# Kernel tuning notes

Measured on AMD Instinct MI355X. Metric: run time of the kernel, lower is better.

The kernel has to match this reference:

```python
import jax, jax.numpy as jnp
import numpy as np

NFILTS = 6  # module-level global in the original repo


def setup_inputs() -> dict:
    key = jax.random.key(0)
    k = jax.random.split(key, 6)
    N, T, D, E = 128, 256, 10, NFILTS
    merged = jax.random.normal(k[0], (N, T, 14), dtype=jnp.float32)
    y_pred_i = jax.random.normal(k[1], (N, T, E), dtype=jnp.float32)
    y_pred_ij = jax.random.normal(k[2], (N, N, T, E), dtype=jnp.float32)
    # input1 holds flux errors in channels [1+nfilts : -2]; keep them bounded away from 0
    input1 = jax.random.uniform(k[3], (N, T, 1 + E + E + 2), dtype=jnp.float32) + 0.5
    samples = jax.random.normal(k[4], (N, D), dtype=jnp.float32)
    labels = jax.random.randint(k[5], (N,), 0, 10, dtype=jnp.int64)
    return {"merged": merged, "y_pred_i": y_pred_i, "y_pred_ij": y_pred_ij,
            "input1": input1, "samples": samples, "labels": labels}


def reference(merged, y_pred_i, y_pred_ij, input1, samples, labels):
    # err_true: [N, T, E]
    err_true = input1[:, :, 1 + NFILTS:-2]
    # pairwise latent distance: S_ij[i,j] = mean_d (samples[j] - samples[i])^2 -> [N, N]
    d = samples[None, :, :] - samples[:, None, :]
    S_ij = jnp.mean(d * d, axis=-1)
    # second term: mean over (T, E) of (y_pred_ij[i,j] - y_pred_i[j])^2 / err_true[j]^2 / 10
    diffsq = jnp.square(y_pred_ij - y_pred_i[None, :, :, :])          # [N, N, T, E]
    second = jnp.mean(diffsq / jnp.square(err_true)[None], axis=(2, 3)) / 10.0  # [N, N]
    avg_term = 0.5 * (second + second.T)
    L_sim = jnp.mean(jnp.abs(S_ij - avg_term))
    return L_sim
```

## Files before the change

kernel.cpp:

```cpp
#include <hip/hip_runtime.h>

#define NN 128
#define TT 256
#define EE 6
#define DD 10
#define TE (TT*EE)
#define C1 15

typedef float f32x4 __attribute__((ext_vector_type(4)));

__global__ __launch_bounds__(256) void pair_all(const float* __restrict__ yij,
                                                const float* __restrict__ yi,
                                                const float* __restrict__ input1,
                                                float* __restrict__ raw,
                                                float* __restrict__ out) {
    const int bid = blockIdx.x;
    const int tid = threadIdx.x;
    const int j   = bid & (NN - 1);

    if (bid == 0 && tid == 0) out[0] = 0.0f;

    __shared__ f32x4 w4[TE / 4];
    float* wl = (float*)w4;
    const float* __restrict__ i1 = input1 + (size_t)j * TT * C1 + 1 + EE;
    for (int k = tid; k < TE; k += 256) {
        const int t = k / EE, e = k - t * EE;
        const float v = i1[t * C1 + e];
        wl[k] = 1.0f / (v * v);
    }
    __syncthreads();

    const int lane = tid & 63;
    const int tile = (tid >> 6) * (NN * NN / 4) + bid;

    const f32x4* __restrict__ a = (const f32x4*)(yij + (size_t)tile * TE);
    const f32x4* __restrict__ m = (const f32x4*)(yi  + (size_t)j * TE);

    float s0 = 0.0f, s1 = 0.0f, s2 = 0.0f, s3 = 0.0f;
#pragma unroll
    for (int k = 0; k < 6; ++k) {
        const int f = lane + k * 64;
        f32x4 x  = __builtin_nontemporal_load(&a[f]);
        f32x4 mm = m[f];
        f32x4 ww = w4[f];
        float d0 = x.x - mm.x; s0 += d0 * d0 * ww.x;
        float d1 = x.y - mm.y; s1 += d1 * d1 * ww.y;
        float d2 = x.z - mm.z; s2 += d2 * d2 * ww.z;
        float d3 = x.w - mm.w; s3 += d3 * d3 * ww.w;
    }
    float s = (s0 + s1) + (s2 + s3);
#pragma unroll
    for (int off = 32; off > 0; off >>= 1) s += __shfl_down(s, off);
    if (lane == 0) raw[tile] = s;
}

__global__ __launch_bounds__(256) void finalize(const float* __restrict__ raw,
                                                const float* __restrict__ samples,
                                                float* __restrict__ out) {
    __shared__ float smp[DD * NN];
    for (int k = threadIdx.x; k < NN * DD; k += 256) {
        int n = k / DD, d = k % DD;
        smp[d * NN + n] = samples[k];
    }
    __syncthreads();

    const int p = blockIdx.x * 256 + threadIdx.x;
    const int i = p >> 7, j = p & (NN - 1);

    float S = 0.0f;
#pragma unroll
    for (int d = 0; d < DD; ++d) {
        float dd = smp[d * NN + j] - smp[d * NN + i];
        S += dd * dd;
    }
    const float sec = (raw[p] + raw[(j << 7) | i]) * (0.5f / (TE * 10.0f));
    float v = fabsf(S * (1.0f / DD) - sec);

#pragma unroll
    for (int off = 32; off > 0; off >>= 1) v += __shfl_down(v, off);

    __shared__ float ls[4];
    const int tid = threadIdx.x;
    if ((tid & 63) == 0) ls[tid >> 6] = v;
    __syncthreads();
    if (tid == 0)
        atomicAdd(out, (ls[0] + ls[1] + ls[2] + ls[3]) * (1.0f / (NN * NN)));
}

extern "C" void kernel_launch(void* const* d_in, const int* in_sizes, int n_in,
                              void* d_out, int out_size, void* d_ws, size_t ws_size,
                              hipStream_t stream) {
    const float* y_pred_i  = (const float*)d_in[1];
    const float* y_pred_ij = (const float*)d_in[2];
    const float* input1    = (const float*)d_in[3];
    const float* samples   = (const float*)d_in[4];
    float* out = (float*)d_out;

    float* raw = (float*)d_ws;

    pair_all<<<NN * NN / 4, 256, 0, stream>>>(y_pred_ij, y_pred_i, input1, raw, out);
    finalize<<<64, 256, 0, stream>>>(raw, samples, out);
}
```

Measured before the change: 158.6 us.

## Process four i-rows per wave and keep weights/yi in registers

Each wave now handles four (i,j) tiles sharing the same j, and the per-j inverse-squared error weights and y_pred_i slice are loaded once into registers. This replaces the shared-memory weight staging and its barrier. The grid shrinks from 4096 to 1024 blocks. Each block therefore amortizes the input1/yi loads and division over 16 tiles instead of 4, at the cost of more registers and fewer blocks in flight for a bandwidth-bound stream.

```diff
diff --git a/kernel.cpp b/kernel.cpp
--- a/kernel.cpp
+++ b/kernel.cpp
@@ -14,44 +14,55 @@
                                                 const float* __restrict__ input1,
                                                 float* __restrict__ raw,
                                                 float* __restrict__ out) {
-    const int bid = blockIdx.x;
-    const int tid = threadIdx.x;
-    const int j   = bid & (NN - 1);
+    const int bid  = blockIdx.x;
+    const int tid  = threadIdx.x;
+    const int lane = tid & 63;
+    const int wv   = tid >> 6;
+    const int j    = bid & (NN - 1);
+    const int i0   = (bid >> 7) * 16 + wv * 4;
 
     if (bid == 0 && tid == 0) out[0] = 0.0f;
 
-    __shared__ f32x4 w4[TE / 4];
-    float* wl = (float*)w4;
+    f32x4 wj[6], mj[6];
     const float* __restrict__ i1 = input1 + (size_t)j * TT * C1 + 1 + EE;
-    for (int k = tid; k < TE; k += 256) {
-        const int t = k / EE, e = k - t * EE;
-        const float v = i1[t * C1 + e];
-        wl[k] = 1.0f / (v * v);
-    }
-    __syncthreads();
-
-    const int lane = tid & 63;
-    const int tile = (tid >> 6) * (NN * NN / 4) + bid;
-
-    const f32x4* __restrict__ a = (const f32x4*)(yij + (size_t)tile * TE);
-    const f32x4* __restrict__ m = (const f32x4*)(yi  + (size_t)j * TE);
-
-    float s0 = 0.0f, s1 = 0.0f, s2 = 0.0f, s3 = 0.0f;
 #pragma unroll
     for (int k = 0; k < 6; ++k) {
-        const int f = lane + k * 64;
-        f32x4 x  = __builtin_nontemporal_load(&a[f]);
-        f32x4 mm = m[f];
-        f32x4 ww = w4[f];
-        float d0 = x.x - mm.x; s0 += d0 * d0 * ww.x;
-        float d1 = x.y - mm.y; s1 += d1 * d1 * ww.y;
-        float d2 = x.z - mm.z; s2 += d2 * d2 * ww.z;
-        float d3 = x.w - mm.w; s3 += d3 * d3 * ww.w;
+        mj[k] = *(const f32x4*)(yi + (size_t)j * TE + 4 * lane + 256 * k);
+        f32x4 t;
+#pragma unroll
+        for (int c = 0; c < 4; ++c) {
+            const int idx = 4 * lane + c + 256 * k;
+            const int tt  = idx / EE, e = idx - tt * EE;
+            const float v = i1[tt * C1 + e];
+            t[c] = 1.0f / (v * v);
+        }
+        wj[k] = t;
     }
-    float s = (s0 + s1) + (s2 + s3);
+
+    float accs[4];
 #pragma unroll
-    for (int off = 32; off > 0; off >>= 1) s += __shfl_down(s, off);
-    if (lane == 0) raw[tile] = s;
+    for (int p = 0; p < 4; ++p) {
+        const f32x4* __restrict__ a =
+            (const f32x4*)(yij + ((size_t)(i0 + p) * NN + j) * TE);
+        float s0 = 0.0f, s1 = 0.0f, s2 = 0.0f, s3 = 0.0f;
+#pragma unroll
+        for (int k = 0; k < 6; ++k) {
+            f32x4 x = __builtin_nontemporal_load(&a[lane + 64 * k]);
+            float d0 = x.x - mj[k].x; s0 += d0 * d0 * wj[k].x;
+            float d1 = x.y - mj[k].y; s1 += d1 * d1 * wj[k].y;
+            float d2 = x.z - mj[k].z; s2 += d2 * d2 * wj[k].z;
+            float d3 = x.w - mj[k].w; s3 += d3 * d3 * wj[k].w;
+        }
+        accs[p] = (s0 + s1) + (s2 + s3);
+    }
+
+#pragma unroll
+    for (int p = 0; p < 4; ++p) {
+        float s = accs[p];
+#pragma unroll
+        for (int off = 32; off > 0; off >>= 1) s += __shfl_down(s, off);
+        if (lane == 0) raw[(i0 + p) * NN + j] = s;
+    }
 }
 
 __global__ __launch_bounds__(256) void finalize(const float* __restrict__ raw,
@@ -98,6 +109,6 @@
 
     float* raw = (float*)d_ws;
 
-    pair_all<<<NN * NN / 4, 256, 0, stream>>>(y_pred_ij, y_pred_i, input1, raw, out);
+    pair_all<<<1024, 256, 0, stream>>>(y_pred_ij, y_pred_i, input1, raw, out);
     finalize<<<64, 256, 0, stream>>>(raw, samples, out);
 }
```

Result: no change. 155.6 us, median of 2 (-1.8%).
